# Kernel optimization log

Hardware: AMD Instinct MI355X
Metric: run time of the kernel (lower is better)

The kernel has to match this reference:

```python
import jax, jax.numpy as jnp
import numpy as np
import math

N_EXP = 64
TOP_K = 2
EVAL_CAPACITY = 1.25
MIN_CAPACITY = 4


def _capacity(num_tokens):
    cap = math.floor(TOP_K * EVAL_CAPACITY * num_tokens / N_EXP)
    cap += cap % 2
    return max(cap, MIN_CAPACITY)


def setup_inputs() -> dict:
    key = jax.random.key(0)
    k1, k2 = jax.random.split(key)
    x = jax.random.normal(k1, (4096, 2048), dtype=jnp.float32)
    w_g = jax.random.normal(k2, (64, 2048), dtype=jnp.float32) * 0.02
    return {"x": x, "w_g": w_g}


def reference(x, w_g):
    # x: [T, D], w_g: [E, D]
    T, D = x.shape
    cap = _capacity(T)

    logits = x @ w_g.T                                   # [T, E]
    top_v, top_i = jax.lax.top_k(logits, TOP_K)          # [T, K]

    # softmax over only the top-k logits (others -> -inf)
    rows = jnp.arange(T)[:, None]
    masked = jnp.full_like(logits, -jnp.inf).at[rows, top_i].set(top_v)
    router_probs = jax.nn.softmax(masked, axis=-1)       # [T, E]

    # Capacity-aware assignment: flatten (token, k) pairs in row-major order,
    # exactly matching the original sequential double loop. The slot for each
    # attempt is the exclusive prefix count of attempts to that expert; once an
    # expert's count exceeds capacity, all later attempts are rejected, which
    # matches the sequential semantics (usage only stops growing at capacity).
    flat_e = top_i.reshape(-1)                           # [T*K]
    tok = jnp.repeat(jnp.arange(T), TOP_K)               # [T*K]
    onehot = jax.nn.one_hot(flat_e, N_EXP, dtype=jnp.int32)   # [T*K, E]
    cum = jnp.cumsum(onehot, axis=0)                     # inclusive counts
    slot = cum[jnp.arange(T * TOP_K), flat_e] - 1        # exclusive prefix count
    assigned = slot < cap

    used_capacity = jnp.minimum(cum[-1], cap).astype(jnp.int32)   # [E]

    # Route rejected attempts to a scratch slot `cap`, then slice it off.
    safe_slot = jnp.where(assigned, slot, cap)
    w = router_probs[tok, flat_e]                        # [T*K]

    cb_weight = (jnp.zeros((T, N_EXP, cap + 1), dtype=x.dtype)
                 .at[tok, flat_e, safe_slot].set(w))[..., :cap]
    sec_mask = (jnp.zeros((T, N_EXP, cap + 1), dtype=bool)
                .at[tok, flat_e, safe_slot].set(True))[..., :cap]

    return used_capacity, cb_weight, sec_mask
```

## Files before the change

### kernel.cpp

```cpp
#include <hip/hip_runtime.h>
#include <math.h>

#define T_TOK 4096
#define D_DIM 2048
#define NEXP  64
#define CAP   160

#define TPB   4
#define NGB   (T_TOK / TPB)
#define NZB   2048

typedef float vfloat4 __attribute__((ext_vector_type(4)));

__global__ __launch_bounds__(256) void fused_main(
    const float* __restrict__ x, const float* __restrict__ wg,
    float* __restrict__ out, int out_size,
    int* __restrict__ topi, float* __restrict__ topw)
{
    const int bid = blockIdx.x;
    const int tid = threadIdx.x;

    if (bid >= NGB) {
        const int zb = bid - NGB;
        const size_t n4 = (size_t)out_size >> 2;
        vfloat4* o4 = (vfloat4*)out;
        const vfloat4 z = {0.f, 0.f, 0.f, 0.f};
        const size_t stride = (size_t)NZB * 256;
        for (size_t i = (size_t)zb * 256 + tid; i < n4; i += stride)
            __builtin_nontemporal_store(z, &o4[i]);
        if (zb == 0 && tid == 0) {
            for (size_t i = n4 << 2; i < (size_t)out_size; ++i) out[i] = 0.f;
        }
        return;
    }

    const int e    = tid & 63;
    const int w    = __builtin_amdgcn_readfirstlane(tid >> 6);
    const int tok0 = bid * TPB;
    const int wk0  = w * (D_DIM / 4);

    float acc[TPB] = {0.f, 0.f, 0.f, 0.f};

    const float* __restrict__ wrow = wg + (size_t)e * D_DIM + wk0;

    for (int c = 0; c < (D_DIM / 4) / 32; ++c) {
        vfloat4 b[8];
#pragma unroll
        for (int j = 0; j < 8; ++j)
            b[j] = *(const vfloat4*)(wrow + c * 32 + j * 4);
#pragma unroll
        for (int t = 0; t < TPB; ++t) {
            const float* __restrict__ xp =
                x + (size_t)(tok0 + t) * D_DIM + wk0 + c * 32;
            float s = 0.f;
#pragma unroll
            for (int j = 0; j < 8; ++j) {
                s += xp[j*4+0] * b[j].x + xp[j*4+1] * b[j].y
                   + xp[j*4+2] * b[j].z + xp[j*4+3] * b[j].w;
            }
            acc[t] += s;
        }
    }

    __shared__ float sAcc[4][TPB][NEXP];
#pragma unroll
    for (int t = 0; t < TPB; ++t)
        sAcc[w][t][e] = acc[t];
    __syncthreads();

    const int t = w;
    float v = sAcc[0][t][e] + sAcc[1][t][e] + sAcc[2][t][e] + sAcc[3][t][e];

    float v1 = v;         int i1 = e;
    float v2 = -INFINITY; int i2 = NEXP;
#pragma unroll
    for (int off = 32; off >= 1; off >>= 1) {
        const float ov1 = __shfl_xor(v1, off, 64);
        const int   oi1 = __shfl_xor(i1, off, 64);
        const float ov2 = __shfl_xor(v2, off, 64);
        const int   oi2 = __shfl_xor(i2, off, 64);
        const bool firstMine = (v1 > ov1) || (v1 == ov1 && i1 < oi1);
        const float n1  = firstMine ? v1  : ov1;
        const int   ni1 = firstMine ? i1  : oi1;
        const float c1  = firstMine ? ov1 : v1;
        const int   ci1 = firstMine ? oi1 : i1;
        const float c2  = firstMine ? v2  : ov2;
        const int   ci2 = firstMine ? i2  : oi2;
        const bool secondC1 = (c1 > c2) || (c1 == c2 && ci1 < ci2);
        v1 = n1;                      i1 = ni1;
        v2 = secondC1 ? c1 : c2;      i2 = secondC1 ? ci1 : ci2;
    }

    if (e == 0) {
        const int gt = tok0 + t;
        const float r  = expf(v2 - v1);
        const float s1 = 1.0f / (1.0f + r);
        topi[2 * gt + 0] = i1;
        topi[2 * gt + 1] = i2;
        topw[2 * gt + 0] = s1;
        topw[2 * gt + 1] = r * s1;
    }
}

__global__ __launch_bounds__(64) void scatter_assign(
    const int* __restrict__ topi, const float* __restrict__ topw,
    float* __restrict__ out)
{
    __shared__ int cnt[NEXP];
    const int lane = threadIdx.x;
    cnt[lane] = 0;
    __syncthreads();

    float* __restrict__ cb   = out + NEXP;
    float* __restrict__ mask = out + NEXP + (size_t)T_TOK * NEXP * CAP;

    const unsigned long long lt = ((unsigned long long)1 << lane) - 1ull;
    const int NCH = (T_TOK * 2) / 64;

    int   e  = topi[lane];
    float tw = topw[lane];

    for (int c = 0; c < NCH; ++c) {
        int   en  = 0;
        float twn = 0.f;
        if (c + 1 < NCH) {
            en  = topi[(c + 1) * 64 + lane];
            twn = topw[(c + 1) * 64 + lane];
        }

        unsigned long long m = ~0ull;
#pragma unroll
        for (int b = 0; b < 6; ++b) {
            const unsigned long long vb = __ballot((e >> b) & 1);
            m &= ((e >> b) & 1) ? vb : ~vb;
        }
        const int p     = __popcll(m & lt);
        const int base  = cnt[e];
        const int slot  = base + p;
        if (p == 0) cnt[e] = base + __popcll(m);

        if (slot < CAP) {
            const int f = c * 64 + lane;
            const int t = f >> 1;
            const size_t off = ((size_t)t * NEXP + e) * CAP + slot;
            cb[off]   = tw;
            mask[off] = 1.0f;
        }
        e = en; tw = twn;
    }

    int used = cnt[lane];
    if (used > CAP) used = CAP;
    out[lane] = (float)used;
}

extern "C" void kernel_launch(void* const* d_in, const int* in_sizes, int n_in,
                              void* d_out, int out_size, void* d_ws, size_t ws_size,
                              hipStream_t stream)
{
    const float* x  = (const float*)d_in[0];
    const float* wg = (const float*)d_in[1];
    float* out = (float*)d_out;

    int*   topi = (int*)d_ws;
    float* topw = (float*)(topi + T_TOK * 2);

    fused_main<<<NGB + NZB, 256, 0, stream>>>(x, wg, out, out_size, topi, topw);
    scatter_assign<<<1, 64, 0, stream>>>(topi, topw, out);
}
```

Before: 456.5 us.

## Parallelize capacity scatter with one wavefront per expert

Replaces the single-wavefront sequential scatter, which matched experts via six ballots and shared-memory counters, with 64 wavefronts that each own one expert. Each wave ballots for its expert and keeps a running prefix count in a register. This removes the serial dependency chain and the shared-memory round trips per chunk. The cost is that every wave rereads the full top-k index and weight arrays.

```diff
diff --git a/kernel.cpp b/kernel.cpp
--- a/kernel.cpp
+++ b/kernel.cpp
@@ -102,23 +102,22 @@
     }
 }
 
-__global__ __launch_bounds__(64) void scatter_assign(
+__global__ __launch_bounds__(256) void scatter_assign(
     const int* __restrict__ topi, const float* __restrict__ topw,
     float* __restrict__ out)
 {
-    __shared__ int cnt[NEXP];
-    const int lane = threadIdx.x;
-    cnt[lane] = 0;
-    __syncthreads();
+    const int lane = threadIdx.x & 63;
+    const int myE  = (blockIdx.x << 2) | (threadIdx.x >> 6);
 
     float* __restrict__ cb   = out + NEXP;
-    float* __restrict__ mask = out + NEXP + (size_t)T_TOK * NEXP * CAP;
+    float* __restrict__ mask = cb + (size_t)T_TOK * NEXP * CAP;
 
     const unsigned long long lt = ((unsigned long long)1 << lane) - 1ull;
     const int NCH = (T_TOK * 2) / 64;
 
     int   e  = topi[lane];
     float tw = topw[lane];
+    int   running = 0;
 
     for (int c = 0; c < NCH; ++c) {
         int   en  = 0;
@@ -128,30 +127,25 @@
             twn = topw[(c + 1) * 64 + lane];
         }
 
-        unsigned long long m = ~0ull;
-#pragma unroll
-        for (int b = 0; b < 6; ++b) {
-            const unsigned long long vb = __ballot((e >> b) & 1);
-            m &= ((e >> b) & 1) ? vb : ~vb;
+        const unsigned long long m = __ballot(e == myE);
+        if (e == myE) {
+            const int slot = running + __popcll(m & lt);
+            if (slot < CAP) {
+                const int t = (c * 64 + lane) >> 1;
+                const size_t off = ((size_t)t * NEXP + myE) * CAP + slot;
+                cb[off]   = tw;
+                mask[off] = 1.0f;
+            }
         }
-        const int p     = __popcll(m & lt);
-        const int base  = cnt[e];
-        const int slot  = base + p;
-        if (p == 0) cnt[e] = base + __popcll(m);
+        running += __popcll(m);
 
-        if (slot < CAP) {
-            const int f = c * 64 + lane;
-            const int t = f >> 1;
-            const size_t off = ((size_t)t * NEXP + e) * CAP + slot;
-            cb[off]   = tw;
-            mask[off] = 1.0f;
-        }
         e = en; tw = twn;
     }
 
-    int used = cnt[lane];
-    if (used > CAP) used = CAP;
-    out[lane] = (float)used;
+    if (lane == 0) {
+        const int used = running < CAP ? running : CAP;
+        out[myE] = (float)used;
+    }
 }
 
 extern "C" void kernel_launch(void* const* d_in, const int* in_sizes, int n_in,
@@ -166,5 +160,5 @@
     float* topw = (float*)(topi + T_TOK * 2);
 
     fused_main<<<NGB + NZB, 256, 0, stream>>>(x, wg, out, out_size, topi, topw);
-    scatter_assign<<<1, 64, 0, stream>>>(topi, topw, out);
+    scatter_assign<<<16, 256, 0, stream>>>(topi, topw, out);
 }
```

Result: faster. 435.3 us (-4.6%).
